# Performance work log

Measured on AMD Instinct MI355X. Metric: run time of the kernel, lower is better.

The kernel has to match this reference:

```python
import jax, jax.numpy as jnp
import numpy as np

N, L2, C = 4096, 49, 128   # lmax=6 -> (lmax+1)**2 = 49
RES = 18                   # grid resolution (beta, alpha)


def setup_inputs() -> dict:
    key = jax.random.key(0)
    k1, k2, k3 = jax.random.split(key, 3)
    inputs = jax.random.normal(k1, (N, L2, C), dtype=jnp.float32)
    # Stand-ins for the precomputed spherical-harmonic transform matrices
    # (to_grid_mat / from_grid_mat), shape (res_beta, res_alpha, (lmax+1)**2).
    W_to = jax.random.normal(k2, (RES, RES, L2), dtype=jnp.float32) / jnp.sqrt(jnp.float32(L2))
    W_from = jax.random.normal(k3, (RES, RES, L2), dtype=jnp.float32) / jnp.sqrt(jnp.float32(RES * RES))
    return {"inputs": inputs, "W_to": W_to, "W_from": W_from}


def reference(inputs, W_to, W_from):
    # to_grid: coefficients -> real-space S2 grid  (n, beta, alpha, c)
    grid = jnp.einsum('bai,nic->nbac', W_to, inputs)
    # elementwise self tensor product on the grid
    grid = grid * grid
    # from_grid: project back to spherical-harmonic coefficients (n, i, c)
    outputs = jnp.einsum('bai,nbac->nic', W_from, grid)
    return outputs
```

## Files before the change

### kernel.cpp

```cpp
#include <hip/hip_runtime.h>


#define NN    4096
#define L2D   49
#define CCH   128
#define GTOT  324
#define KC2   11

typedef __attribute__((ext_vector_type(8)))  short bf16x8;
typedef __attribute__((ext_vector_type(16))) float f32x16;

#define WT_SHORTS (KC2 * 4 * 64 * 8)
#define WF_SHORTS (2 * KC2 * 2 * 64 * 8)

__device__ __forceinline__ short f2bf(float f) {
    union { float f; unsigned u; } x; x.f = f;
    return (short)((x.u + 0x7fffu + ((x.u >> 16) & 1u)) >> 16);
}

__device__ __forceinline__ unsigned cvtpk(float lo, float hi) {
    unsigned r;
    asm("v_cvt_pk_bf16_f32 %0, %1, %2" : "=v"(r) : "v"(lo), "v"(hi));
    return r;
}

__global__ void prep_w_kernel(const float* __restrict__ Wt,
                              const float* __restrict__ Wf,
                              short* __restrict__ WtF,
                              short* __restrict__ WfF)
{
    int idx = blockIdx.x * 256 + threadIdx.x;
    if (idx < WT_SHORTS) {
        int j = idx & 7, lane = (idx >> 3) & 63, ki = (idx >> 9) & 3, kc2 = idx >> 11;
        int m = lane & 31, H = lane >> 5;
        int gwc = ((m >> 3) & 1) * 16 + ((m >> 2) & 1) * 8 + (m >> 4) * 4 + (m & 3);
        int g = kc2 * 32 + gwc;
        int i = ki * 16 + H * 8 + j;
        WtF[idx] = f2bf((g < GTOT && i < L2D) ? Wt[g * L2D + i] : 0.0f);
    } else if (idx < WT_SHORTS + WF_SHORTS) {
        int e = idx - WT_SHORTS;
        int j = e & 7, lane = (e >> 3) & 63, cc = (e >> 9) & 1;
        int u = e >> 10;
        int kc2 = u % KC2, it = u / KC2;
        int m = lane & 31, H = lane >> 5;
        int i = it * 32 + m;
        int g = kc2 * 32 + cc * 16 + H * 8 + j;
        WfF[e] = f2bf((g < GTOT && i < L2D) ? Wf[g * L2D + i] : 0.0f);
    }
}

__global__ __launch_bounds__(256, 3)
void stp_mfma7_kernel(const float* __restrict__ inp,
                      const short* __restrict__ WtF,
                      const short* __restrict__ WfF,
                      float* __restrict__ out)
{
    const int tid  = threadIdx.x;
    const int lane = tid & 63;
    const int wave = tid >> 6;
    const int m    = lane & 31;
    const int H    = lane >> 5;

    const int task = blockIdx.x * 4 + wave;
    const int n    = task >> 1;
    const int h    = task & 1;

    const float* __restrict__ Xn = inp + (size_t)n * (L2D * CCH);

    bf16x8 Bx[2][4];
    #pragma unroll
    for (int cq = 0; cq < 2; ++cq) {
        const int c = h * 64 + cq * 32 + m;
        #pragma unroll
        for (int ki = 0; ki < 4; ++ki) {
            union { bf16x8 v; unsigned u[4]; } b;
            #pragma unroll
            for (int p = 0; p < 4; ++p) {
                const int i0 = ki * 16 + H * 8 + 2 * p;
                float v0 = (i0     < L2D) ? Xn[(i0    ) * CCH + c] : 0.0f;
                float v1 = (i0 + 1 < L2D) ? Xn[(i0 + 1) * CCH + c] : 0.0f;
                b.u[p] = cvtpk(v0, v1);
            }
            Bx[cq][ki] = b.v;
        }
    }

    f32x16 acc2[2][2];
    #pragma unroll
    for (int it = 0; it < 2; ++it)
        #pragma unroll
        for (int cq = 0; cq < 2; ++cq)
            acc2[it][cq] = (f32x16)(0.0f);

    #pragma unroll 1
    for (int kc2 = 0; kc2 < KC2; ++kc2) {
        bf16x8 Wtf[4];
        #pragma unroll
        for (int ki = 0; ki < 4; ++ki)
            Wtf[ki] = *(const bf16x8*)&WtF[((kc2 * 4 + ki) * 64 + lane) * 8];
        bf16x8 Wff[2][2];
        #pragma unroll
        for (int it = 0; it < 2; ++it)
            #pragma unroll
            for (int cc = 0; cc < 2; ++cc)
                Wff[it][cc] = *(const bf16x8*)&WfF[(((it * KC2 + kc2) * 2 + cc) * 64 + lane) * 8];

        #pragma unroll
        for (int cq = 0; cq < 2; ++cq) {
            f32x16 g = (f32x16)(0.0f);
            #pragma unroll
            for (int ki = 0; ki < 4; ++ki)
                g = __builtin_amdgcn_mfma_f32_32x32x16_bf16(Wtf[ki], Bx[cq][ki], g, 0, 0, 0);

            union { bf16x8 v; unsigned u[4]; } bg0, bg1;
            bg0.u[0] = cvtpk(g[0] * g[0],   g[1] * g[1]);
            bg0.u[1] = cvtpk(g[2] * g[2],   g[3] * g[3]);
            bg0.u[2] = cvtpk(g[8] * g[8],   g[9] * g[9]);
            bg0.u[3] = cvtpk(g[10] * g[10], g[11] * g[11]);
            bg1.u[0] = cvtpk(g[4] * g[4],   g[5] * g[5]);
            bg1.u[1] = cvtpk(g[6] * g[6],   g[7] * g[7]);
            bg1.u[2] = cvtpk(g[12] * g[12], g[13] * g[13]);
            bg1.u[3] = cvtpk(g[14] * g[14], g[15] * g[15]);

            #pragma unroll
            for (int it = 0; it < 2; ++it) {
                acc2[it][cq] = __builtin_amdgcn_mfma_f32_32x32x16_bf16(Wff[it][0], bg0.v, acc2[it][cq], 0, 0, 0);
                acc2[it][cq] = __builtin_amdgcn_mfma_f32_32x32x16_bf16(Wff[it][1], bg1.v, acc2[it][cq], 0, 0, 0);
            }
        }
    }

    float* __restrict__ On = out + (size_t)n * (L2D * CCH);
    #pragma unroll
    for (int it = 0; it < 2; ++it) {
        #pragma unroll
        for (int cq = 0; cq < 2; ++cq) {
            const int c = h * 64 + cq * 32 + m;
            #pragma unroll
            for (int r = 0; r < 16; ++r) {
                const int i = it * 32 + (r & 3) + 8 * (r >> 2) + 4 * H;
                if (i < L2D) On[i * CCH + c] = acc2[it][cq][r];
            }
        }
    }
}

extern "C" void kernel_launch(void* const* d_in, const int* in_sizes, int n_in,
                              void* d_out, int out_size, void* d_ws, size_t ws_size,
                              hipStream_t stream) {
    const float* inp = (const float*)d_in[0];
    const float* Wt  = (const float*)d_in[1];
    const float* Wf  = (const float*)d_in[2];
    float* out = (float*)d_out;

    short* WtF = (short*)d_ws;
    short* WfF = WtF + WT_SHORTS;

    const int prep_threads = WT_SHORTS + WF_SHORTS;
    prep_w_kernel<<<(prep_threads + 255) / 256, 256, 0, stream>>>(Wt, Wf, WtF, WfF);
    stp_mfma7_kernel<<<2048, 256, 0, stream>>>(inp, WtF, WfF, out);
}
```

Baseline: 210.6 us.

## Split waves into producer and consumer roles pipelined through LDS

Each block now handles two tasks instead of four. Two producer waves compute the to-grid MFMAs and the squaring, then write bf16 grid tiles into a double-buffered shared-memory array. Two consumer waves read those tiles one step later and run the from-grid MFMAs. The goal is to overlap the two GEMM stages and reduce per-wave register pressure, at the cost of a block-wide barrier every iteration, LDS traffic, and twice as many blocks.

```diff
diff --git a/kernel.cpp b/kernel.cpp
--- a/kernel.cpp
+++ b/kernel.cpp
@@ -50,38 +50,44 @@
 }
 
 __global__ __launch_bounds__(256, 3)
-void stp_mfma7_kernel(const float* __restrict__ inp,
+void stp_mfma8_kernel(const float* __restrict__ inp,
                       const short* __restrict__ WtF,
                       const short* __restrict__ WfF,
                       float* __restrict__ out)
 {
+    __shared__ __attribute__((aligned(16))) short sBg[2][2][2][2][64 * 8];
+
     const int tid  = threadIdx.x;
     const int lane = tid & 63;
     const int wave = tid >> 6;
     const int m    = lane & 31;
     const int H    = lane >> 5;
 
-    const int task = blockIdx.x * 4 + wave;
+    const bool prod = wave < 2;
+    const int  tl   = prod ? wave : wave - 2;
+
+    const int task = blockIdx.x * 2 + tl;
     const int n    = task >> 1;
     const int h    = task & 1;
 
-    const float* __restrict__ Xn = inp + (size_t)n * (L2D * CCH);
-
     bf16x8 Bx[2][4];
-    #pragma unroll
-    for (int cq = 0; cq < 2; ++cq) {
-        const int c = h * 64 + cq * 32 + m;
+    if (prod) {
+        const float* __restrict__ Xn = inp + (size_t)n * (L2D * CCH);
         #pragma unroll
-        for (int ki = 0; ki < 4; ++ki) {
-            union { bf16x8 v; unsigned u[4]; } b;
+        for (int cq = 0; cq < 2; ++cq) {
+            const int c = h * 64 + cq * 32 + m;
             #pragma unroll
-            for (int p = 0; p < 4; ++p) {
-                const int i0 = ki * 16 + H * 8 + 2 * p;
-                float v0 = (i0     < L2D) ? Xn[(i0    ) * CCH + c] : 0.0f;
-                float v1 = (i0 + 1 < L2D) ? Xn[(i0 + 1) * CCH + c] : 0.0f;
-                b.u[p] = cvtpk(v0, v1);
+            for (int ki = 0; ki < 4; ++ki) {
+                union { bf16x8 v; unsigned u[4]; } b;
+                #pragma unroll
+                for (int p = 0; p < 4; ++p) {
+                    const int i0 = ki * 16 + H * 8 + 2 * p;
+                    float v0 = (i0     < L2D) ? Xn[(i0    ) * CCH + c] : 0.0f;
+                    float v1 = (i0 + 1 < L2D) ? Xn[(i0 + 1) * CCH + c] : 0.0f;
+                    b.u[p] = cvtpk(v0, v1);
+                }
+                Bx[cq][ki] = b.v;
             }
-            Bx[cq][ki] = b.v;
         }
     }
 
@@ -93,53 +99,72 @@
             acc2[it][cq] = (f32x16)(0.0f);
 
     #pragma unroll 1
-    for (int kc2 = 0; kc2 < KC2; ++kc2) {
-        bf16x8 Wtf[4];
-        #pragma unroll
-        for (int ki = 0; ki < 4; ++ki)
-            Wtf[ki] = *(const bf16x8*)&WtF[((kc2 * 4 + ki) * 64 + lane) * 8];
-        bf16x8 Wff[2][2];
-        #pragma unroll
-        for (int it = 0; it < 2; ++it)
-            #pragma unroll
-            for (int cc = 0; cc < 2; ++cc)
-                Wff[it][cc] = *(const bf16x8*)&WfF[(((it * KC2 + kc2) * 2 + cc) * 64 + lane) * 8];
+    for (int k = 0; k <= KC2; ++k) {
+        if (prod) {
+            if (k < KC2) {
+                bf16x8 Wtf[4];
+                #pragma unroll
+                for (int ki = 0; ki < 4; ++ki)
+                    Wtf[ki] = *(const bf16x8*)&WtF[((k * 4 + ki) * 64 + lane) * 8];
 
-        #pragma unroll
-        for (int cq = 0; cq < 2; ++cq) {
-            f32x16 g = (f32x16)(0.0f);
-            #pragma unroll
-            for (int ki = 0; ki < 4; ++ki)
-                g = __builtin_amdgcn_mfma_f32_32x32x16_bf16(Wtf[ki], Bx[cq][ki], g, 0, 0, 0);
+                #pragma unroll
+                for (int cq = 0; cq < 2; ++cq) {
+                    f32x16 g = (f32x16)(0.0f);
+                    #pragma unroll
+                    for (int ki = 0; ki < 4; ++ki)
+                        g = __builtin_amdgcn_mfma_f32_32x32x16_bf16(Wtf[ki], Bx[cq][ki], g, 0, 0, 0);
 
-            union { bf16x8 v; unsigned u[4]; } bg0, bg1;
-            bg0.u[0] = cvtpk(g[0] * g[0],   g[1] * g[1]);
-            bg0.u[1] = cvtpk(g[2] * g[2],   g[3] * g[3]);
-            bg0.u[2] = cvtpk(g[8] * g[8],   g[9] * g[9]);
-            bg0.u[3] = cvtpk(g[10] * g[10], g[11] * g[11]);
-            bg1.u[0] = cvtpk(g[4] * g[4],   g[5] * g[5]);
-            bg1.u[1] = cvtpk(g[6] * g[6],   g[7] * g[7]);
-            bg1.u[2] = cvtpk(g[12] * g[12], g[13] * g[13]);
-            bg1.u[3] = cvtpk(g[14] * g[14], g[15] * g[15]);
+                    union { bf16x8 v; unsigned u[4]; } bg0, bg1;
+                    bg0.u[0] = cvtpk(g[0] * g[0],   g[1] * g[1]);
+                    bg0.u[1] = cvtpk(g[2] * g[2],   g[3] * g[3]);
+                    bg0.u[2] = cvtpk(g[8] * g[8],   g[9] * g[9]);
+                    bg0.u[3] = cvtpk(g[10] * g[10], g[11] * g[11]);
+                    bg1.u[0] = cvtpk(g[4] * g[4],   g[5] * g[5]);
+                    bg1.u[1] = cvtpk(g[6] * g[6],   g[7] * g[7]);
+                    bg1.u[2] = cvtpk(g[12] * g[12], g[13] * g[13]);
+                    bg1.u[3] = cvtpk(g[14] * g[14], g[15] * g[15]);
 
-            #pragma unroll
-            for (int it = 0; it < 2; ++it) {
-                acc2[it][cq] = __builtin_amdgcn_mfma_f32_32x32x16_bf16(Wff[it][0], bg0.v, acc2[it][cq], 0, 0, 0);
-                acc2[it][cq] = __builtin_amdgcn_mfma_f32_32x32x16_bf16(Wff[it][1], bg1.v, acc2[it][cq], 0, 0, 0);
+                    *(bf16x8*)&sBg[k & 1][tl][cq][0][lane * 8] = bg0.v;
+                    *(bf16x8*)&sBg[k & 1][tl][cq][1][lane * 8] = bg1.v;
+                }
+            }
+        } else {
+            if (k >= 1) {
+                const int kc2 = k - 1;
+                bf16x8 Wff[2][2];
+                #pragma unroll
+                for (int it = 0; it < 2; ++it)
+                    #pragma unroll
+                    for (int cc = 0; cc < 2; ++cc)
+                        Wff[it][cc] = *(const bf16x8*)&WfF[(((it * KC2 + kc2) * 2 + cc) * 64 + lane) * 8];
+
+                #pragma unroll
+                for (int cq = 0; cq < 2; ++cq) {
+                    bf16x8 bgr0 = *(const bf16x8*)&sBg[kc2 & 1][tl][cq][0][lane * 8];
+                    bf16x8 bgr1 = *(const bf16x8*)&sBg[kc2 & 1][tl][cq][1][lane * 8];
+                    #pragma unroll
+                    for (int it = 0; it < 2; ++it) {
+                        acc2[it][cq] = __builtin_amdgcn_mfma_f32_32x32x16_bf16(Wff[it][0], bgr0, acc2[it][cq], 0, 0, 0);
+                        acc2[it][cq] = __builtin_amdgcn_mfma_f32_32x32x16_bf16(Wff[it][1], bgr1, acc2[it][cq], 0, 0, 0);
+                    }
+                }
             }
         }
+        __syncthreads();
     }
 
-    float* __restrict__ On = out + (size_t)n * (L2D * CCH);
-    #pragma unroll
-    for (int it = 0; it < 2; ++it) {
+    if (!prod) {
+        float* __restrict__ On = out + (size_t)n * (L2D * CCH);
         #pragma unroll
-        for (int cq = 0; cq < 2; ++cq) {
-            const int c = h * 64 + cq * 32 + m;
+        for (int it = 0; it < 2; ++it) {
             #pragma unroll
-            for (int r = 0; r < 16; ++r) {
-                const int i = it * 32 + (r & 3) + 8 * (r >> 2) + 4 * H;
-                if (i < L2D) On[i * CCH + c] = acc2[it][cq][r];
+            for (int cq = 0; cq < 2; ++cq) {
+                const int c = h * 64 + cq * 32 + m;
+                #pragma unroll
+                for (int r = 0; r < 16; ++r) {
+                    const int i = it * 32 + (r & 3) + 8 * (r >> 2) + 4 * H;
+                    if (i < L2D) On[i * CCH + c] = acc2[it][cq][r];
+                }
             }
         }
     }
@@ -158,5 +183,5 @@
 
     const int prep_threads = WT_SHORTS + WF_SHORTS;
     prep_w_kernel<<<(prep_threads + 255) / 256, 256, 0, stream>>>(Wt, Wf, WtF, WfF);
-    stp_mfma7_kernel<<<2048, 256, 0, stream>>>(inp, WtF, WfF, out);
+    stp_mfma8_kernel<<<4096, 256, 0, stream>>>(inp, WtF, WfF, out);
 }
```

After: 243.4 us. +15.5%, slower.

## Stage input tile through swizzled LDS with float4 loads, read B fragments from shared

Applied to the files above, without the earlier changes.

Each block now cooperatively loads two input rows with coalesced float4 global reads, converts them to bf16, and stores them transposed into a padded, XOR-swizzled LDS buffer. Each wave then reads its MFMA B fragments from LDS inside the kernel loop instead of keeping them in registers after strided scalar global loads. This targets poor global load coalescing and register pressure, with the launch bound raised to 4 blocks per SIMD. In exchange it adds a block barrier, LDS usage, scalar 2-byte LDS stores that may bank-conflict, and LDS reads repeated on every kc2 iteration.

```diff
diff --git a/kernel.cpp b/kernel.cpp
--- a/kernel.cpp
+++ b/kernel.cpp
@@ -7,6 +7,9 @@
 #define GTOT  324
 #define KC2   11
 
+#define XSTR  68
+
+typedef __attribute__((ext_vector_type(4)))  short short4v;
 typedef __attribute__((ext_vector_type(8)))  short bf16x8;
 typedef __attribute__((ext_vector_type(16))) float f32x16;
 
@@ -49,41 +52,62 @@
     }
 }
 
-__global__ __launch_bounds__(256, 3)
-void stp_mfma7_kernel(const float* __restrict__ inp,
-                      const short* __restrict__ WtF,
-                      const short* __restrict__ WfF,
-                      float* __restrict__ out)
+__global__ __launch_bounds__(256, 4)
+void stp_mfma10_kernel(const float* __restrict__ inp,
+                       const short* __restrict__ WtF,
+                       const short* __restrict__ WfF,
+                       float* __restrict__ out)
 {
+    __shared__ __attribute__((aligned(16))) short sXT[2][CCH * XSTR];
+
     const int tid  = threadIdx.x;
     const int lane = tid & 63;
     const int wave = tid >> 6;
-    const int m    = lane & 31;
-    const int H    = lane >> 5;
 
-    const int task = blockIdx.x * 4 + wave;
-    const int n    = task >> 1;
-    const int h    = task & 1;
+    const int n0 = blockIdx.x * 2;
 
-    const float* __restrict__ Xn = inp + (size_t)n * (L2D * CCH);
-
-    bf16x8 Bx[2][4];
-    #pragma unroll
-    for (int cq = 0; cq < 2; ++cq) {
-        const int c = h * 64 + cq * 32 + m;
-        #pragma unroll
-        for (int ki = 0; ki < 4; ++ki) {
-            union { bf16x8 v; unsigned u[4]; } b;
-            #pragma unroll
-            for (int p = 0; p < 4; ++p) {
-                const int i0 = ki * 16 + H * 8 + 2 * p;
-                float v0 = (i0     < L2D) ? Xn[(i0    ) * CCH + c] : 0.0f;
-                float v1 = (i0 + 1 < L2D) ? Xn[(i0 + 1) * CCH + c] : 0.0f;
-                b.u[p] = cvtpk(v0, v1);
-            }
-            Bx[cq][ki] = b.v;
+    #pragma unroll 4
+    for (int pass = 0; pass < 16; ++pass) {
+        const int q   = pass * 256 + tid;
+        const int c4i = q & 31;
+        const int i   = (q >> 5) & 63;
+        const int nb  = q >> 11;
+        short v0 = 0, v1 = 0, v2 = 0, v3 = 0;
+        if (i < L2D) {
+            const float4 x = *(const float4*)&inp[((size_t)(n0 + nb) * L2D + i) * CCH + c4i * 4];
+            v0 = f2bf(x.x); v1 = f2bf(x.y); v2 = f2bf(x.z); v3 = f2bf(x.w);
+        }
+        const int s8b = i >> 2;
+        const int il  = i & 3;
+        short* dst = &sXT[nb][0];
+        {
+            const int c = c4i * 4 + 0;
+            dst[c * XSTR + ((s8b ^ ((c >> 4) & 1)) << 2) + il] = v0;
+        }
+        {
+            const int c = c4i * 4 + 1;
+            dst[c * XSTR + ((s8b ^ ((c >> 4) & 1)) << 2) + il] = v1;
+        }
+        {
+            const int c = c4i * 4 + 2;
+            dst[c * XSTR + ((s8b ^ ((c >> 4) & 1)) << 2) + il] = v2;
+        }
+        {
+            const int c = c4i * 4 + 3;
+            dst[c * XSTR + ((s8b ^ ((c >> 4) & 1)) << 2) + il] = v3;
         }
     }
+    __syncthreads();
+
+    const int m  = lane & 31;
+    const int H  = lane >> 5;
+    const int sw = (m >> 4) & 1;
+
+    const int nb = wave >> 1;
+    const int h  = wave & 1;
+    const int n  = n0 + nb;
+
+    const short* __restrict__ xb = &sXT[nb][0];
 
     f32x16 acc2[2][2];
     #pragma unroll
@@ -107,10 +131,18 @@
 
         #pragma unroll
         for (int cq = 0; cq < 2; ++cq) {
+            const int cl = h * 64 + cq * 32 + m;
             f32x16 g = (f32x16)(0.0f);
             #pragma unroll
-            for (int ki = 0; ki < 4; ++ki)
-                g = __builtin_amdgcn_mfma_f32_32x32x16_bf16(Wtf[ki], Bx[cq][ki], g, 0, 0, 0);
+            for (int ki = 0; ki < 4; ++ki) {
+                union { bf16x8 v; short4v q[2]; } b;
+                #pragma unroll
+                for (int jh = 0; jh < 2; ++jh) {
+                    const int s8 = (ki * 4 + H * 2 + jh) ^ sw;
+                    b.q[jh] = *(const short4v*)&xb[cl * XSTR + s8 * 4];
+                }
+                g = __builtin_amdgcn_mfma_f32_32x32x16_bf16(Wtf[ki], b.v, g, 0, 0, 0);
+            }
 
             union { bf16x8 v; unsigned u[4]; } bg0, bg1;
             bg0.u[0] = cvtpk(g[0] * g[0],   g[1] * g[1]);
@@ -158,5 +190,5 @@
 
     const int prep_threads = WT_SHORTS + WF_SHORTS;
     prep_w_kernel<<<(prep_threads + 255) / 256, 256, 0, stream>>>(Wt, Wf, WtF, WfF);
-    stp_mfma7_kernel<<<2048, 256, 0, stream>>>(inp, WtF, WfF, out);
+    stp_mfma10_kernel<<<2048, 256, 0, stream>>>(inp, WtF, WfF, out);
 }
```

New measurement: 240.3 us. 14.1% more time.
